# Optimization experiments

Measured on AMD Instinct MI355X. Metric: run time of the kernel, lower is better.

## Reference

```python
import jax, jax.numpy as jnp
import numpy as np

E, H, F, LE, LD, K, CD, DIN = 256, 8, 1024, 4, 3, 8, 4, 4
B, S = 16, 512
SIG2 = 1.0 ** 2 + 1e-8   # dr_sigma**2 + 1e-8
EPS = 1e-5               # LayerNorm / BatchNorm eps


def _ln(x, w, b):
    m = x.mean(-1, keepdims=True)
    v = ((x - m) ** 2).mean(-1, keepdims=True)
    return (x - m) / jnp.sqrt(v + EPS) * w + b


def _gelu(x):
    return jax.nn.gelu(x, approximate=False)  # torch nn.GELU default = exact erf


def _mha(xq, xkv, qkv_w, qkv_b, out_w, out_b, bias=None):
    # torch nn.MultiheadAttention (batch_first), additive float attn bias broadcast over heads
    wq, wk, wv = jnp.split(qkv_w, 3, axis=0)
    bq, bk, bv = jnp.split(qkv_b, 3)
    q = xq @ wq.T + bq
    k = xkv @ wk.T + bk
    v = xkv @ wv.T + bv
    Bn, Tq, Tk = q.shape[0], q.shape[1], k.shape[1]
    hd = E // H
    qh = q.reshape(Bn, Tq, H, hd)
    kh = k.reshape(Bn, Tk, H, hd)
    vh = v.reshape(Bn, Tk, H, hd)
    s = jnp.einsum('bqhd,bkhd->bhqk', qh, kh) / jnp.sqrt(jnp.asarray(hd, q.dtype))
    if bias is not None:
        s = s + bias[:, None]  # same bias for every head
    p = jax.nn.softmax(s, axis=-1)
    o = jnp.einsum('bhqk,bkhd->bqhd', p, vh).reshape(Bn, Tq, E)
    return o @ out_w.T + out_b


def _forward(x, mask, parent_idx, in_w, in_b, bn_w, bn_b, dr_gamma,
             e_qkv_w, e_qkv_b, e_out_w, e_out_b, e_l1_w, e_l1_b, e_l2_w, e_l2_b,
             e_n1_w, e_n1_b, e_n2_w, e_n2_b,
             parent_w, parent_b, query_embed, c1_w, c1_b, c2_w, c2_b,
             d_sqkv_w, d_sqkv_b, d_sout_w, d_sout_b,
             d_cqkv_w, d_cqkv_b, d_cout_w, d_cout_b,
             d_l1_w, d_l1_b, d_l2_w, d_l2_b,
             d_n1_w, d_n1_b, d_n2_w, d_n2_b, d_n3_w, d_n3_b,
             child_w, child_b, o1_w, o1_b, o2_w, o2_b):
    x = jnp.nan_to_num(x)
    # input_dim==4 convention: (log_pt, dEta, dPhi, log_E)
    coords = jnp.stack([x[..., 1], x[..., 2]], axis=-1)          # [B,S,2]
    # input_proj: Linear -> BatchNorm1d (eval: mean 0, var 1) -> GELU (dropout=identity in eval)
    h = x @ in_w.T + in_b
    h = (h / jnp.sqrt(1.0 + EPS)) * bn_w + bn_b
    h = _gelu(h)
    # dR Gaussian attention bias: [B,S,S]; mask is all-valid so no -inf fill
    d = coords[:, :, None, :] - coords[:, None, :, :]
    dr2 = d[..., 0] ** 2 + d[..., 1] ** 2
    bias = -(dr_gamma[0] * dr2) / (2.0 * SIG2)
    # dR-biased pre-norm encoder
    for i in range(LE):
        hn = _ln(h, e_n1_w[i], e_n1_b[i])
        h = h + _mha(hn, hn, e_qkv_w[i], e_qkv_b[i], e_out_w[i], e_out_b[i], bias)
        hn = _ln(h, e_n2_w[i], e_n2_b[i])
        h = h + _gelu(hn @ e_l1_w[i].T + e_l1_b[i]) @ e_l2_w[i].T + e_l2_b[i]
    memory = jnp.nan_to_num(h)
    parent_logit = (memory @ parent_w.T + parent_b)[..., 0]       # [B,S]
    # conditional decoder queries
    p = memory[jnp.arange(memory.shape[0]), parent_idx]           # [B,E]
    m = mask.astype(memory.dtype)
    g = (memory * m[..., None]).sum(1) / jnp.maximum(m.sum(1, keepdims=True), 1.0)
    cond = _gelu(jnp.concatenate([p, g], -1) @ c1_w.T + c1_b) @ c2_w.T + c2_b
    t = query_embed[None] + cond[:, None]                         # [B,K,E]
    # pre-norm transformer decoder (self-attn, cross-attn, ff)
    for i in range(LD):
        tn = _ln(t, d_n1_w[i], d_n1_b[i])
        t = t + _mha(tn, tn, d_sqkv_w[i], d_sqkv_b[i], d_sout_w[i], d_sout_b[i])
        tn = _ln(t, d_n2_w[i], d_n2_b[i])
        t = t + _mha(tn, memory, d_cqkv_w[i], d_cqkv_b[i], d_cout_w[i], d_cout_b[i])
        tn = _ln(t, d_n3_w[i], d_n3_b[i])
        t = t + _gelu(tn @ d_l1_w[i].T + d_l1_b[i]) @ d_l2_w[i].T + d_l2_b[i]
    child_feat = t @ child_w.T + child_b                          # [B,K,CD]
    obj_logit = (_gelu(t @ o1_w.T + o1_b) @ o2_w.T + o2_b)[..., 0]  # [B,K]
    return parent_logit, child_feat, obj_logit


def setup_inputs() -> dict:
    key = jax.random.key(0)
    ks = iter(jax.random.split(key, 64))
    def w(shape, scale=0.05):
        return jax.random.normal(next(ks), shape, jnp.float32) * scale
    return {
        'x': jax.random.normal(next(ks), (B, S, DIN), jnp.float32),
        'mask': jnp.ones((B, S), dtype=bool),
        'parent_idx': jax.random.randint(next(ks), (B,), 0, S),
        'in_w': w((E, DIN)), 'in_b': jnp.zeros((E,)),
        'bn_w': jnp.ones((E,)), 'bn_b': jnp.zeros((E,)),
        'dr_gamma': jnp.ones((1,)),
        'e_qkv_w': w((LE, 3 * E, E)), 'e_qkv_b': jnp.zeros((LE, 3 * E)),
        'e_out_w': w((LE, E, E)), 'e_out_b': jnp.zeros((LE, E)),
        'e_l1_w': w((LE, F, E)), 'e_l1_b': jnp.zeros((LE, F)),
        'e_l2_w': w((LE, E, F)), 'e_l2_b': jnp.zeros((LE, E)),
        'e_n1_w': jnp.ones((LE, E)), 'e_n1_b': jnp.zeros((LE, E)),
        'e_n2_w': jnp.ones((LE, E)), 'e_n2_b': jnp.zeros((LE, E)),
        'parent_w': w((1, E)), 'parent_b': jnp.zeros((1,)),
        'query_embed': w((K, E), 0.02),
        'c1_w': w((E, 2 * E)), 'c1_b': jnp.zeros((E,)),
        'c2_w': w((E, E)), 'c2_b': jnp.zeros((E,)),
        'd_sqkv_w': w((LD, 3 * E, E)), 'd_sqkv_b': jnp.zeros((LD, 3 * E)),
        'd_sout_w': w((LD, E, E)), 'd_sout_b': jnp.zeros((LD, E)),
        'd_cqkv_w': w((LD, 3 * E, E)), 'd_cqkv_b': jnp.zeros((LD, 3 * E)),
        'd_cout_w': w((LD, E, E)), 'd_cout_b': jnp.zeros((LD, E)),
        'd_l1_w': w((LD, F, E)), 'd_l1_b': jnp.zeros((LD, F)),
        'd_l2_w': w((LD, E, F)), 'd_l2_b': jnp.zeros((LD, E)),
        'd_n1_w': jnp.ones((LD, E)), 'd_n1_b': jnp.zeros((LD, E)),
        'd_n2_w': jnp.ones((LD, E)), 'd_n2_b': jnp.zeros((LD, E)),
        'd_n3_w': jnp.ones((LD, E)), 'd_n3_b': jnp.zeros((LD, E)),
        'child_w': w((CD, E)), 'child_b': jnp.zeros((CD,)),
        'o1_w': w((E, E)), 'o1_b': jnp.zeros((E,)),
        'o2_w': w((1, E)), 'o2_b': jnp.zeros((1,)),
    }


def reference(x, mask, parent_idx, in_w, in_b, bn_w, bn_b, dr_gamma,
              e_qkv_w, e_qkv_b, e_out_w, e_out_b, e_l1_w, e_l1_b, e_l2_w, e_l2_b,
              e_n1_w, e_n1_b, e_n2_w, e_n2_b,
              parent_w, parent_b, query_embed, c1_w, c1_b, c2_w, c2_b,
              d_sqkv_w, d_sqkv_b, d_sout_w, d_sout_b,
              d_cqkv_w, d_cqkv_b, d_cout_w, d_cout_b,
              d_l1_w, d_l1_b, d_l2_w, d_l2_b,
              d_n1_w, d_n1_b, d_n2_w, d_n2_b, d_n3_w, d_n3_b,
              child_w, child_b, o1_w, o1_b, o2_w, o2_b):
    return _forward(x, mask, parent_idx, in_w, in_b, bn_w, bn_b, dr_gamma,
                    e_qkv_w, e_qkv_b, e_out_w, e_out_b, e_l1_w, e_l1_b, e_l2_w, e_l2_b,
                    e_n1_w, e_n1_b, e_n2_w, e_n2_b,
                    parent_w, parent_b, query_embed, c1_w, c1_b, c2_w, c2_b,
                    d_sqkv_w, d_sqkv_b, d_sout_w, d_sout_b,
                    d_cqkv_w, d_cqkv_b, d_cout_w, d_cout_b,
                    d_l1_w, d_l1_b, d_l2_w, d_l2_b,
                    d_n1_w, d_n1_b, d_n2_w, d_n2_b, d_n3_w, d_n3_b,
                    child_w, child_b, o1_w, o1_b, o2_w, o2_b)
```

## Files before the change

kernel.cpp:

```cpp
#include <hip/hip_runtime.h>
#include <math.h>

#define E 256
#define H 8
#define HD 32
#define FF 1024
#define LE 4
#define LDN 3
#define KQ 8
#define CDIM 4
#define DIN 4
#define BATCH 16
#define SEQ 512

typedef __attribute__((ext_vector_type(8))) short s8b;
typedef __attribute__((ext_vector_type(4))) float f32x4;

__device__ __forceinline__ float gelu_f(float x) {
  return 0.5f * x * (1.f + erff(x * 0.70710678118654752f));
}

__device__ __forceinline__ unsigned short f2b(float f) {
  union { float f; unsigned u; } a;
  a.f = f;
  unsigned r = (a.u + 0x7fffu + ((a.u >> 16) & 1u)) >> 16;
  return (unsigned short)r;
}

__device__ __forceinline__ float b2f(unsigned short u) {
  union { unsigned u; float f; } a;
  a.u = ((unsigned)u) << 16;
  return a.f;
}

__device__ __forceinline__ void gload16(const unsigned short* g, unsigned short* l) {
  __builtin_amdgcn_global_load_lds((const __attribute__((address_space(1))) void*)g,
                                   (__attribute__((address_space(3))) void*)l, 16, 0, 0);
}

template <int GELU, int RESID, int OMODE>
__global__ __launch_bounds__(256) void mfma_gemm_kernel(
    const unsigned short* __restrict__ A, const unsigned short* __restrict__ Wt,
    const float* __restrict__ bias, const float* __restrict__ resid,
    float* __restrict__ outf, unsigned short* __restrict__ outb,
    unsigned short* __restrict__ vtb,
    int M, int N, int K) {
  __shared__ __align__(16) unsigned short As[128 * 32];
  __shared__ __align__(16) unsigned short Bs[128 * 32];
  int tid = threadIdx.x;
  int lane = tid & 63, w = tid >> 6;
  int row0 = blockIdx.y * 128, col0 = blockIdx.x * 128;
  int wr = (w >> 1) * 64, wc = (w & 1) * 64;
  f32x4 acc[4][4] = {};

  int sr0 = w * 32 + (lane >> 2);
  int sr1 = sr0 + 16;
  int sc = lane & 3;
  int gc0 = (sc ^ ((sr0 >> 1) & 3)) * 8;
  int gc1 = (sc ^ ((sr1 >> 1) & 3)) * 8;
  const unsigned short* Ap0 = A + (size_t)(row0 + sr0) * K + gc0;
  const unsigned short* Ap1 = A + (size_t)(row0 + sr1) * K + gc1;
  const unsigned short* Bp0 = Wt + (size_t)(col0 + sr0) * K + gc0;
  const unsigned short* Bp1 = Wt + (size_t)(col0 + sr1) * K + gc1;
  unsigned short* lA0 = As + (w * 32) * 32;
  unsigned short* lA1 = As + (w * 32 + 16) * 32;
  unsigned short* lB0 = Bs + (w * 32) * 32;
  unsigned short* lB1 = Bs + (w * 32 + 16) * 32;

  for (int k0 = 0; k0 < K; k0 += 32) {
    __syncthreads();
    gload16(Ap0 + k0, lA0);
    gload16(Ap1 + k0, lA1);
    gload16(Bp0 + k0, lB0);
    gload16(Bp1 + k0, lB1);
    __syncthreads();
    int krow = lane & 15, kq = lane >> 4;
    s8b afr[4], bfr[4];
    #pragma unroll
    for (int mi = 0; mi < 4; ++mi) {
      int r = wr + mi * 16 + krow;
      afr[mi] = *(const s8b*)(As + r * 32 + ((kq ^ ((r >> 1) & 3)) * 8));
    }
    #pragma unroll
    for (int ni = 0; ni < 4; ++ni) {
      int r = wc + ni * 16 + krow;
      bfr[ni] = *(const s8b*)(Bs + r * 32 + ((kq ^ ((r >> 1) & 3)) * 8));
    }
    #pragma unroll
    for (int mi = 0; mi < 4; ++mi)
      #pragma unroll
      for (int ni = 0; ni < 4; ++ni)
        acc[mi][ni] = __builtin_amdgcn_mfma_f32_16x16x32_bf16(afr[mi], bfr[ni], acc[mi][ni], 0, 0, 0);
  }

  int cl = lane & 15, rb = (lane >> 4) * 4;
  #pragma unroll
  for (int ni = 0; ni < 4; ++ni) {
    int col = col0 + wc + ni * 16 + cl;
    float bv = bias[col];
    #pragma unroll
    for (int mi = 0; mi < 4; ++mi) {
      #pragma unroll
      for (int j = 0; j < 4; ++j) {
        int row = row0 + wr + mi * 16 + rb + j;
        float v = acc[mi][ni][j] + bv;
        if (RESID) v += resid[(size_t)row * N + col];
        if (GELU) v = gelu_f(v);
        if (OMODE == 0) {
          outf[(size_t)row * N + col] = v;
        } else if (OMODE == 1) {
          outb[(size_t)row * N + col] = f2b(v);
        } else {
          int b = row >> 9, s = row & 511;
          int sect = col >> 8, hh = (col >> 5) & 7, d = col & 31;
          if (sect < 2)
            outb[((((size_t)sect * BATCH + b) * H + hh) * SEQ + s) * HD + d] = f2b(v);
          else
            vtb[(((size_t)b * H + hh) * HD + d) * SEQ + s] = f2b(v);
        }
      }
    }
  }
}

__global__ __launch_bounds__(256) void mfma_gemm64_kernel(
    const unsigned short* __restrict__ A, const unsigned short* __restrict__ Wt,
    const float* __restrict__ bias, const float* __restrict__ resid,
    float* __restrict__ outf, int M, int N, int K) {
  __shared__ __align__(16) unsigned short As[64 * 32];
  __shared__ __align__(16) unsigned short Bs[128 * 32];
  int tid = threadIdx.x;
  int lane = tid & 63, w = tid >> 6;
  int row0 = blockIdx.y * 64, col0 = blockIdx.x * 128;
  int wr = (w >> 1) * 32, wc = (w & 1) * 64;
  f32x4 acc[2][4] = {};

  int sc = lane & 3;
  int srA = w * 16 + (lane >> 2);
  int gcA = (sc ^ ((srA >> 1) & 3)) * 8;
  const unsigned short* ApA = A + (size_t)(row0 + srA) * K + gcA;
  unsigned short* lA = As + (w * 16) * 32;
  int sr0 = w * 32 + (lane >> 2);
  int sr1 = sr0 + 16;
  int gc0 = (sc ^ ((sr0 >> 1) & 3)) * 8;
  int gc1 = (sc ^ ((sr1 >> 1) & 3)) * 8;
  const unsigned short* Bp0 = Wt + (size_t)(col0 + sr0) * K + gc0;
  const unsigned short* Bp1 = Wt + (size_t)(col0 + sr1) * K + gc1;
  unsigned short* lB0 = Bs + (w * 32) * 32;
  unsigned short* lB1 = Bs + (w * 32 + 16) * 32;

  for (int k0 = 0; k0 < K; k0 += 32) {
    __syncthreads();
    gload16(ApA + k0, lA);
    gload16(Bp0 + k0, lB0);
    gload16(Bp1 + k0, lB1);
    __syncthreads();
    int krow = lane & 15, kq = lane >> 4;
    s8b afr[2], bfr[4];
    #pragma unroll
    for (int mi = 0; mi < 2; ++mi) {
      int r = wr + mi * 16 + krow;
      afr[mi] = *(const s8b*)(As + r * 32 + ((kq ^ ((r >> 1) & 3)) * 8));
    }
    #pragma unroll
    for (int ni = 0; ni < 4; ++ni) {
      int r = wc + ni * 16 + krow;
      bfr[ni] = *(const s8b*)(Bs + r * 32 + ((kq ^ ((r >> 1) & 3)) * 8));
    }
    #pragma unroll
    for (int mi = 0; mi < 2; ++mi)
      #pragma unroll
      for (int ni = 0; ni < 4; ++ni)
        acc[mi][ni] = __builtin_amdgcn_mfma_f32_16x16x32_bf16(afr[mi], bfr[ni], acc[mi][ni], 0, 0, 0);
  }

  int cl = lane & 15, rb = (lane >> 4) * 4;
  #pragma unroll
  for (int ni = 0; ni < 4; ++ni) {
    int col = col0 + wc + ni * 16 + cl;
    float bv = bias[col];
    #pragma unroll
    for (int mi = 0; mi < 2; ++mi) {
      #pragma unroll
      for (int j = 0; j < 4; ++j) {
        int row = row0 + wr + mi * 16 + rb + j;
        float v = acc[mi][ni][j] + bv + resid[(size_t)row * N + col];
        outf[(size_t)row * N + col] = v;
      }
    }
  }
}

__global__ __launch_bounds__(256) void mfma_attn_kernel(
    const unsigned short* __restrict__ qkb, const unsigned short* __restrict__ vt,
    const float2* __restrict__ carr, const float* __restrict__ gamma_p,
    unsigned short* __restrict__ out) {
  __shared__ __align__(16) unsigned short P[4][16 * 64];
  int tid = threadIdx.x, lane = tid & 63, w = tid >> 6;
  int qt = blockIdx.x, h = blockIdx.y, b = blockIdx.z;
  int q0 = qt * 64 + w * 16;
  const unsigned short* qh = qkb + (((size_t)b * H + h) * SEQ) * HD;
  const unsigned short* kh = qkb + ((((size_t)BATCH + b) * H + h) * SEQ) * HD;
  const unsigned short* vh = vt + (((size_t)b * H + h) * HD) * SEQ;
  int r16 = lane & 15, q4 = lane >> 4;
  s8b qa = *(const s8b*)(qh + (size_t)(q0 + r16) * HD + q4 * 8);
  float eq[4], pq[4];
  #pragma unroll
  for (int j = 0; j < 4; ++j) {
    float2 c = carr[b * SEQ + q0 + q4 * 4 + j];
    eq[j] = c.x; pq[j] = c.y;
  }
  float gam = gamma_p[0] * 0.49999999500000004f;
  const float scale = 0.17677669529663687f;
  float m[4], lsum[4];
  #pragma unroll
  for (int j = 0; j < 4; ++j) { m[j] = -1e30f; lsum[j] = 0.f; }
  f32x4 o0 = {}, o1 = {};
  const f32x4 zf = {0.f, 0.f, 0.f, 0.f};
  unsigned short* pw = &P[w][0];

  for (int t = 0; t < SEQ / 64; ++t) {
    int k0 = t * 64;
    f32x4 sf[4];
    #pragma unroll
    for (int f = 0; f < 4; ++f) {
      s8b bk = *(const s8b*)(kh + (size_t)(k0 + f * 16 + r16) * HD + q4 * 8);
      sf[f] = __builtin_amdgcn_mfma_f32_16x16x32_bf16(qa, bk, zf, 0, 0, 0);
    }
    float ek[4], pk[4];
    #pragma unroll
    for (int f = 0; f < 4; ++f) {
      float2 c = carr[b * SEQ + k0 + f * 16 + r16];
      ek[f] = c.x; pk[f] = c.y;
    }
    float sc_[4][4];
    float tmax[4] = {-1e30f, -1e30f, -1e30f, -1e30f};
    #pragma unroll
    for (int f = 0; f < 4; ++f)
      #pragma unroll
      for (int j = 0; j < 4; ++j) {
        float de = eq[j] - ek[f], dp = pq[j] - pk[f];
        float v = sf[f][j] * scale - gam * (de * de + dp * dp);
        sc_[f][j] = v;
        tmax[j] = fmaxf(tmax[j], v);
      }
    #pragma unroll
    for (int j = 0; j < 4; ++j) {
      #pragma unroll
      for (int off = 1; off < 16; off <<= 1)
        tmax[j] = fmaxf(tmax[j], __shfl_xor(tmax[j], off));
      float mn = fmaxf(m[j], tmax[j]);
      float al = __expf(m[j] - mn);
      m[j] = mn;
      lsum[j] *= al;
      o0[j] *= al;
      o1[j] *= al;
    }
    __syncthreads();
    #pragma unroll
    for (int f = 0; f < 4; ++f)
      #pragma unroll
      for (int j = 0; j < 4; ++j) {
        float p = __expf(sc_[f][j] - m[j]);
        lsum[j] += p;
        int prow = q4 * 4 + j;
        int c = f * 16 + r16;
        int chunk = (c >> 3) ^ (prow & 7);
        pw[prow * 64 + chunk * 8 + (c & 7)] = f2b(p);
      }
    __syncthreads();
    #pragma unroll
    for (int ks = 0; ks < 2; ++ks) {
      int chunk = (ks * 4 + q4) ^ (r16 & 7);
      s8b pa = *(const s8b*)(pw + r16 * 64 + chunk * 8);
      s8b v0 = *(const s8b*)(vh + (size_t)r16 * SEQ + k0 + ks * 32 + q4 * 8);
      s8b v1 = *(const s8b*)(vh + (size_t)(16 + r16) * SEQ + k0 + ks * 32 + q4 * 8);
      o0 = __builtin_amdgcn_mfma_f32_16x16x32_bf16(pa, v0, o0, 0, 0, 0);
      o1 = __builtin_amdgcn_mfma_f32_16x16x32_bf16(pa, v1, o1, 0, 0, 0);
    }
  }
  #pragma unroll
  for (int j = 0; j < 4; ++j) {
    #pragma unroll
    for (int off = 1; off < 16; off <<= 1)
      lsum[j] += __shfl_xor(lsum[j], off);
    float inv = 1.f / lsum[j];
    size_t rbase = ((size_t)(b * SEQ + q0 + q4 * 4 + j)) * E + h * HD;
    out[rbase + r16] = f2b(o0[j] * inv);
    out[rbase + 16 + r16] = f2b(o1[j] * inv);
  }
}

__global__ void coords_kernel(const float* __restrict__ x, float2* __restrict__ carr) {
  int i = blockIdx.x * 256 + threadIdx.x;
  if (i >= BATCH * SEQ) return;
  carr[i] = make_float2(x[(size_t)i * DIN + 1], x[(size_t)i * DIN + 2]);
}

__global__ void f2b_kernel(const float* __restrict__ in, unsigned short* __restrict__ out, int n4) {
  int i = blockIdx.x * 256 + threadIdx.x;
  if (i >= n4) return;
  float4 v = ((const float4*)in)[i];
  ushort4 o;
  o.x = f2b(v.x); o.y = f2b(v.y); o.z = f2b(v.z); o.w = f2b(v.w);
  ((ushort4*)out)[i] = o;
}

__global__ void kvw_remap_kernel(const float* __restrict__ w, const float* __restrict__ b,
                                 unsigned short* __restrict__ wout, float* __restrict__ bout) {
  int i = blockIdx.x * 256 + threadIdx.x;
  if (i < 1536) bout[i] = b[(i >> 9) * 768 + 256 + (i & 511)];
  if (i >= 98304) return;
  int row = i >> 6, cc = i & 63;
  int l = row >> 9, rr = row & 511;
  const float* src = w + ((size_t)l * 768 + 256 + rr) * 256 + cc * 4;
  float4 v = *(const float4*)src;
  ushort4 o;
  o.x = f2b(v.x); o.y = f2b(v.y); o.z = f2b(v.z); o.w = f2b(v.w);
  *(ushort4*)(wout + (size_t)row * 256 + cc * 4) = o;
}


template <int N, int GELU>
__global__ __launch_bounds__(256) void dec_ln_gemv_kernel(
    const float* __restrict__ t, const float* __restrict__ nw, const float* __restrict__ nb,
    const float* __restrict__ W, const float* __restrict__ bias, float* __restrict__ outg) {
  __shared__ float X[8][256];
  __shared__ float Pp[4][64][9];
  int b = blockIdx.x, by = blockIdx.y, tid = threadIdx.x;
  const float* tg = t + (size_t)b * 2048;
  int w = tid >> 6, l = tid & 63;
  #pragma unroll
  for (int rr = 0; rr < 2; ++rr) {
    int r = w * 2 + rr;
    float v0 = tg[r * 256 + l], v1 = tg[r * 256 + 64 + l];
    float v2 = tg[r * 256 + 128 + l], v3 = tg[r * 256 + 192 + l];
    float s = v0 + v1 + v2 + v3;
    for (int o = 32; o > 0; o >>= 1) s += __shfl_xor(s, o);
    float mean = s * (1.f / 256);
    float d0 = v0 - mean, d1 = v1 - mean, d2 = v2 - mean, d3 = v3 - mean;
    float var = d0 * d0 + d1 * d1 + d2 * d2 + d3 * d3;
    for (int o = 32; o > 0; o >>= 1) var += __shfl_xor(var, o);
    float inv = rsqrtf(var * (1.f / 256) + 1e-5f);
    X[r][l] = d0 * inv * nw[l] + nb[l];
    X[r][l + 64] = d1 * inv * nw[l + 64] + nb[l + 64];
    X[r][l + 128] = d2 * inv * nw[l + 128] + nb[l + 128];
    X[r][l + 192] = d3 * inv * nw[l + 192] + nb[l + 192];
  }
  __syncthreads();
  int j = tid & 63, kq = tid >> 6;
  int col = by * 64 + j;
  const float4* wp = (const float4*)(W + (size_t)col * 256 + kq * 64);
  float acc[8] = {};
  #pragma unroll
  for (int kk = 0; kk < 16; ++kk) {
    float4 wv = wp[kk];
    int base = kq * 64 + kk * 4;
    #pragma unroll
    for (int r = 0; r < 8; ++r) {
      float4 xv = *(const float4*)&X[r][base];
      acc[r] += xv.x * wv.x + xv.y * wv.y + xv.z * wv.z + xv.w * wv.w;
    }
  }
  #pragma unroll
  for (int r = 0; r < 8; ++r) Pp[kq][j][r] = acc[r];
  __syncthreads();
  for (int i = tid; i < 512; i += 256) {
    int r = i & 7, j2 = i >> 3;
    float v = Pp[0][j2][r] + Pp[1][j2][r] + Pp[2][j2][r] + Pp[3][j2][r] + bias[by * 64 + j2];
    if (GELU) v = gelu_f(v);
    outg[((size_t)b * 8 + r) * N + by * 64 + j2] = v;
  }
}

__global__ __launch_bounds__(256) void dec_selfattn_sout_kernel(
    const float* __restrict__ qkvg, const float* __restrict__ W, const float* __restrict__ bias,
    float* __restrict__ t) {
  __shared__ float QK[8][768];
  __shared__ float S[512];
  __shared__ float X[8][256];
  __shared__ float Pp[4][64][9];
  int b = blockIdx.x, by = blockIdx.y, tid = threadIdx.x;
  const float* qg = qkvg + (size_t)b * 8 * 768;
  for (int i = tid; i < 6144; i += 256) ((float*)QK)[i] = qg[i];
  __syncthreads();
  for (int t2 = tid; t2 < 512; t2 += 256) {
    int h = t2 >> 6, q = (t2 >> 3) & 7, k = t2 & 7;
    const float* qp = &QK[q][h * 32];
    const float* kp = &QK[k][256 + h * 32];
    float d = 0.f;
    #pragma unroll
    for (int jj = 0; jj < 32; ++jj) d += qp[jj] * kp[jj];
    S[t2] = d * 0.17677669529663687f;
  }
  __syncthreads();
  if (tid < 64) {
    float* row = &S[tid * 8];
    float m = row[0];
    #pragma unroll
    for (int k = 1; k < 8; ++k) m = fmaxf(m, row[k]);
    float sum = 0.f;
    #pragma unroll
    for (int k = 0; k < 8; ++k) { float e = __expf(row[k] - m); row[k] = e; sum += e; }
    float inv = 1.f / sum;
    #pragma unroll
    for (int k = 0; k < 8; ++k) row[k] *= inv;
  }
  __syncthreads();
  for (int i = tid; i < 2048; i += 256) {
    int q = i >> 8, c = i & 255, h = c >> 5;
    const float* pr = &S[h * 64 + q * 8];
    float acc = 0.f;
    #pragma unroll
    for (int k = 0; k < 8; ++k) acc += pr[k] * QK[k][512 + c];
    X[q][c] = acc;
  }
  __syncthreads();
  int j = tid & 63, kq = tid >> 6;
  int col = by * 64 + j;
  const float4* wp = (const float4*)(W + (size_t)col * 256 + kq * 64);
  float acc[8] = {};
  #pragma unroll
  for (int kk = 0; kk < 16; ++kk) {
    float4 wv = wp[kk];
    int base = kq * 64 + kk * 4;
    #pragma unroll
    for (int r = 0; r < 8; ++r) {
      float4 xv = *(const float4*)&X[r][base];
      acc[r] += xv.x * wv.x + xv.y * wv.y + xv.z * wv.z + xv.w * wv.w;
    }
  }
  #pragma unroll
  for (int r = 0; r < 8; ++r) Pp[kq][j][r] = acc[r];
  __syncthreads();
  for (int i = tid; i < 512; i += 256) {
    int r = i & 7, j2 = i >> 3;
    float v = Pp[0][j2][r] + Pp[1][j2][r] + Pp[2][j2][r] + Pp[3][j2][r] + bias[by * 64 + j2];
    t[((size_t)b * 8 + r) * 256 + by * 64 + j2] += v;
  }
}

__global__ __launch_bounds__(256) void dec_gemv_resid_kernel(
    const float* __restrict__ Xg, const float* __restrict__ W, const float* __restrict__ bias,
    float* __restrict__ t) {
  __shared__ float X[8][256];
  __shared__ float Pp[4][64][9];
  int b = blockIdx.x, by = blockIdx.y, tid = threadIdx.x;
  const float* xg = Xg + (size_t)b * 2048;
  for (int i = tid; i < 2048; i += 256) ((float*)X)[i] = xg[i];
  __syncthreads();
  int j = tid & 63, kq = tid >> 6;
  int col = by * 64 + j;
  const float4* wp = (const float4*)(W + (size_t)col * 256 + kq * 64);
  float acc[8] = {};
  #pragma unroll
  for (int kk = 0; kk < 16; ++kk) {
    float4 wv = wp[kk];
    int base = kq * 64 + kk * 4;
    #pragma unroll
    for (int r = 0; r < 8; ++r) {
      float4 xv = *(const float4*)&X[r][base];
      acc[r] += xv.x * wv.x + xv.y * wv.y + xv.z * wv.z + xv.w * wv.w;
    }
  }
  #pragma unroll
  for (int r = 0; r < 8; ++r) Pp[kq][j][r] = acc[r];
  __syncthreads();
  for (int i = tid; i < 512; i += 256) {
    int r = i & 7, j2 = i >> 3;
    float v = Pp[0][j2][r] + Pp[1][j2][r] + Pp[2][j2][r] + Pp[3][j2][r] + bias[by * 64 + j2];
    t[((size_t)b * 8 + r) * 256 + by * 64 + j2] += v;
  }
}

__global__ __launch_bounds__(256) void dec_ffn2_kernel(
    const float* __restrict__ MIDg, const float* __restrict__ W, const float* __restrict__ bias,
    float* __restrict__ t) {
  __shared__ float X[8][1024];
  __shared__ float Pp[4][64][9];
  int b = blockIdx.x, by = blockIdx.y, tid = threadIdx.x;
  const float* xg = MIDg + (size_t)b * 8192;
  for (int i = tid; i < 8192; i += 256) ((float*)X)[i] = xg[i];
  __syncthreads();
  int j = tid & 63, kq = tid >> 6;
  int col = by * 64 + j;
  const float4* wp = (const float4*)(W + (size_t)col * 1024 + kq * 256);
  float acc[8] = {};
  #pragma unroll 8
  for (int kk = 0; kk < 64; ++kk) {
    float4 wv = wp[kk];
    int base = kq * 256 + kk * 4;
    #pragma unroll
    for (int r = 0; r < 8; ++r) {
      float4 xv = *(const float4*)&X[r][base];
      acc[r] += xv.x * wv.x + xv.y * wv.y + xv.z * wv.z + xv.w * wv.w;
    }
  }
  #pragma unroll
  for (int r = 0; r < 8; ++r) Pp[kq][j][r] = acc[r];
  __syncthreads();
  for (int i = tid; i < 512; i += 256) {
    int r = i & 7, j2 = i >> 3;
    float v = Pp[0][j2][r] + Pp[1][j2][r] + Pp[2][j2][r] + Pp[3][j2][r] + bias[by * 64 + j2];
    t[((size_t)b * 8 + r) * 256 + by * 64 + j2] += v;
  }
}

__global__ __launch_bounds__(256) void cross_attn_kernel(
    const float* __restrict__ Q, const unsigned short* __restrict__ KV,
    int koff, int voff, float* __restrict__ out) {
  __shared__ float sv[512];
  __shared__ float red[256];
  __shared__ float qv[32];
  __shared__ float pvred[8][32];
  int tid = threadIdx.x;
  int bid = blockIdx.x;
  int q = bid % KQ;
  int h = (bid / KQ) % H;
  int b = bid / (KQ * H);
  if (tid < 32) qv[tid] = Q[((size_t)(b * KQ + q)) * E + h * HD + tid];
  __syncthreads();
  const float scale = 0.17677669529663687f;
  for (int k = tid; k < SEQ; k += 256) {
    const unsigned short* kp = KV + ((size_t)(b * SEQ + k)) * 1536 + koff + h * HD;
    float d = 0.f;
    #pragma unroll
    for (int j4 = 0; j4 < 4; ++j4) {
      s8b kv8 = *(const s8b*)(kp + j4 * 8);
      #pragma unroll
      for (int j = 0; j < 8; ++j)
        d += qv[j4 * 8 + j] * b2f((unsigned short)kv8[j]);
    }
    sv[k] = d * scale;
  }
  __syncthreads();
  float m = -1e30f;
  for (int k = tid; k < SEQ; k += 256) m = fmaxf(m, sv[k]);
  red[tid] = m; __syncthreads();
  for (int s = 128; s > 0; s >>= 1) {
    if (tid < s) red[tid] = fmaxf(red[tid], red[tid + s]);
    __syncthreads();
  }
  m = red[0]; __syncthreads();
  float lsum = 0.f;
  for (int k = tid; k < SEQ; k += 256) { float e = __expf(sv[k] - m); sv[k] = e; lsum += e; }
  red[tid] = lsum; __syncthreads();
  for (int s = 128; s > 0; s >>= 1) {
    if (tid < s) red[tid] += red[tid + s];
    __syncthreads();
  }
  float denom = red[0];
  int d = tid & 31, g = tid >> 5;
  float acc = 0.f;
  for (int k = g; k < SEQ; k += 8)
    acc += sv[k] * b2f(KV[((size_t)(b * SEQ + k)) * 1536 + voff + h * HD + d]);
  pvred[g][d] = acc;
  __syncthreads();
  if (tid < 32) {
    float r = 0.f;
    #pragma unroll
    for (int gg = 0; gg < 8; ++gg) r += pvred[gg][tid];
    out[((size_t)(b * KQ + q)) * E + h * HD + tid] = r / denom;
  }
}

__global__ void ln_bf16_kernel(const float* __restrict__ in, const float* __restrict__ w,
                               const float* __restrict__ b, unsigned short* __restrict__ out) {
  int r = blockIdx.x;
  int l = threadIdx.x;
  const float* p = in + (size_t)r * E;
  float v0 = p[l], v1 = p[l + 64], v2 = p[l + 128], v3 = p[l + 192];
  float s = v0 + v1 + v2 + v3;
  for (int off = 32; off > 0; off >>= 1) s += __shfl_xor(s, off);
  float mean = s * (1.f / E);
  float d0 = v0 - mean, d1 = v1 - mean, d2 = v2 - mean, d3 = v3 - mean;
  float var = d0 * d0 + d1 * d1 + d2 * d2 + d3 * d3;
  for (int off = 32; off > 0; off >>= 1) var += __shfl_xor(var, off);
  float inv = rsqrtf(var * (1.f / E) + 1e-5f);
  unsigned short* o = out + (size_t)r * E;
  o[l]       = f2b(d0 * inv * w[l]       + b[l]);
  o[l + 64]  = f2b(d1 * inv * w[l + 64]  + b[l + 64]);
  o[l + 128] = f2b(d2 * inv * w[l + 128] + b[l + 128]);
  o[l + 192] = f2b(d3 * inv * w[l + 192] + b[l + 192]);
}

__global__ void input_proj_kernel(const float* __restrict__ x, const float* __restrict__ in_w,
                                  const float* __restrict__ in_b, const float* __restrict__ bn_w,
                                  const float* __restrict__ bn_b, float* __restrict__ h) {
  int idx = blockIdx.x * 256 + threadIdx.x;
  int row = idx >> 8, e = idx & 255;
  const float* xr = x + (size_t)row * DIN;
  float v = in_b[e];
  #pragma unroll
  for (int i = 0; i < DIN; ++i) v += xr[i] * in_w[e * DIN + i];
  v = v * (1.0f / sqrtf(1.0f + 1e-5f)) * bn_w[e] + bn_b[e];
  h[idx] = gelu_f(v);
}

__global__ __launch_bounds__(256) void pool_gather_kernel(
    const float* __restrict__ mem, const int* __restrict__ pidx, float* __restrict__ pg) {
  __shared__ float red[8][32];
  int b = blockIdx.x, cy = blockIdx.y, tid = threadIdx.x;
  int c = cy * 32 + (tid & 31), g = tid >> 5;
  float s = 0.f;
  for (int r = g; r < SEQ; r += 8)
    s += mem[((size_t)b * SEQ + r) * E + c];
  red[g][tid & 31] = s;
  __syncthreads();
  if (tid < 32) {
    float t = 0.f;
    #pragma unroll
    for (int g2 = 0; g2 < 8; ++g2) t += red[g2][tid];
    pg[(size_t)b * 512 + 256 + cy * 32 + tid] = t * (1.f / SEQ);
    pg[(size_t)b * 512 + cy * 32 + tid] = mem[((size_t)b * SEQ + pidx[b]) * E + cy * 32 + tid];
  }
}

__global__ void cond_kernel(const float* __restrict__ pg, const float* __restrict__ c1w,
                            const float* __restrict__ c1b, const float* __restrict__ c2w,
                            const float* __restrict__ c2b, const float* __restrict__ qe,
                            float* __restrict__ t) {
  __shared__ float PG[512];
  __shared__ float C1[256];
  int b = blockIdx.x, c = threadIdx.x;
  PG[c] = pg[(size_t)b * 512 + c];
  PG[c + 256] = pg[(size_t)b * 512 + 256 + c];
  __syncthreads();
  const float4* wp = (const float4*)(c1w + (size_t)c * 512);
  float acc = c1b[c];
  #pragma unroll 8
  for (int kk = 0; kk < 128; ++kk) {
    float4 wv = wp[kk];
    int base = kk * 4;
    acc += PG[base] * wv.x + PG[base + 1] * wv.y + PG[base + 2] * wv.z + PG[base + 3] * wv.w;
  }
  C1[c] = gelu_f(acc);
  __syncthreads();
  const float4* wp2 = (const float4*)(c2w + (size_t)c * 256);
  float acc2 = c2b[c];
  #pragma unroll 8
  for (int kk = 0; kk < 64; ++kk) {
    float4 wv = wp2[kk];
    int base = kk * 4;
    acc2 += C1[base] * wv.x + C1[base + 1] * wv.y + C1[base + 2] * wv.z + C1[base + 3] * wv.w;
  }
  #pragma unroll
  for (int k = 0; k < KQ; ++k)
    t[((size_t)b * KQ + k) * E + c] = qe[k * E + c] + acc2;
}

__global__ void head_kernel(const float* __restrict__ t,
                            const float* __restrict__ childw, const float* __restrict__ childb,
                            const float* __restrict__ o1w, const float* __restrict__ o1b,
                            const float* __restrict__ o2w, const float* __restrict__ o2b,
                            float* __restrict__ out_child, float* __restrict__ out_obj) {
  __shared__ float tr[256];
  __shared__ float red[256];
  int r = blockIdx.x, c = threadIdx.x;
  tr[c] = t[(size_t)r * E + c];
  __syncthreads();
  const float4* wp = (const float4*)(o1w + (size_t)c * 256);
  float acc = o1b[c];
  #pragma unroll 8
  for (int kk = 0; kk < 64; ++kk) {
    float4 wv = wp[kk];
    int base = kk * 4;
    acc += tr[base] * wv.x + tr[base + 1] * wv.y + tr[base + 2] * wv.z + tr[base + 3] * wv.w;
  }
  red[c] = gelu_f(acc) * o2w[c];
  __syncthreads();
  for (int s = 128; s > 0; s >>= 1) {
    if (c < s) red[c] += red[c + s];
    __syncthreads();
  }
  if (c == 0) out_obj[r] = red[0] + o2b[0];
  __syncthreads();
  #pragma unroll
  for (int j = 0; j < CDIM; ++j) {
    red[c] = tr[c] * childw[j * E + c];
    __syncthreads();
    for (int s = 128; s > 0; s >>= 1) {
      if (c < s) red[c] += red[c + s];
      __syncthreads();
    }
    if (c == 0) out_child[r * CDIM + j] = red[0] + childb[j];
    __syncthreads();
  }
}

__global__ void rowdot_kernel(const float* __restrict__ A, const float* __restrict__ w,
                              const float* __restrict__ bias, float* __restrict__ out) {
  int r = blockIdx.x, l = threadIdx.x;
  const float* p = A + (size_t)r * E;
  float s = p[l] * w[l] + p[l + 64] * w[l + 64] + p[l + 128] * w[l + 128] + p[l + 192] * w[l + 192];
  for (int off = 32; off > 0; off >>= 1) s += __shfl_xor(s, off);
  if (l == 0) out[r] = s + bias[0];
}

extern "C" void kernel_launch(void* const* d_in, const int* in_sizes, int n_in,
                              void* d_out, int out_size, void* d_ws, size_t ws_size,
                              hipStream_t stream) {
  const float* x          = (const float*)d_in[0];
  const int*   parent_idx = (const int*)d_in[2];
  const float* in_w  = (const float*)d_in[3];
  const float* in_b  = (const float*)d_in[4];
  const float* bn_w  = (const float*)d_in[5];
  const float* bn_b  = (const float*)d_in[6];
  const float* dr_gamma = (const float*)d_in[7];
  const float* e_qkv_w = (const float*)d_in[8];
  const float* e_qkv_b = (const float*)d_in[9];
  const float* e_out_w = (const float*)d_in[10];
  const float* e_out_b = (const float*)d_in[11];
  const float* e_l1_w = (const float*)d_in[12];
  const float* e_l1_b = (const float*)d_in[13];
  const float* e_l2_w = (const float*)d_in[14];
  const float* e_l2_b = (const float*)d_in[15];
  const float* e_n1_w = (const float*)d_in[16];
  const float* e_n1_b = (const float*)d_in[17];
  const float* e_n2_w = (const float*)d_in[18];
  const float* e_n2_b = (const float*)d_in[19];
  const float* parent_w = (const float*)d_in[20];
  const float* parent_b = (const float*)d_in[21];
  const float* query_embed = (const float*)d_in[22];
  const float* c1_w = (const float*)d_in[23];
  const float* c1_b = (const float*)d_in[24];
  const float* c2_w = (const float*)d_in[25];
  const float* c2_b = (const float*)d_in[26];
  const float* d_sqkv_w = (const float*)d_in[27];
  const float* d_sqkv_b = (const float*)d_in[28];
  const float* d_sout_w = (const float*)d_in[29];
  const float* d_sout_b = (const float*)d_in[30];
  const float* d_cqkv_w = (const float*)d_in[31];
  const float* d_cqkv_b = (const float*)d_in[32];
  const float* d_cout_w = (const float*)d_in[33];
  const float* d_cout_b = (const float*)d_in[34];
  const float* d_l1_w = (const float*)d_in[35];
  const float* d_l1_b = (const float*)d_in[36];
  const float* d_l2_w = (const float*)d_in[37];
  const float* d_l2_b = (const float*)d_in[38];
  const float* d_n1_w = (const float*)d_in[39];
  const float* d_n1_b = (const float*)d_in[40];
  const float* d_n2_w = (const float*)d_in[41];
  const float* d_n2_b = (const float*)d_in[42];
  const float* d_n3_w = (const float*)d_in[43];
  const float* d_n3_b = (const float*)d_in[44];
  const float* child_w = (const float*)d_in[45];
  const float* child_b = (const float*)d_in[46];
  const float* o1_w = (const float*)d_in[47];
  const float* o1_b = (const float*)d_in[48];
  const float* o2_w = (const float*)d_in[49];
  const float* o2_b = (const float*)d_in[50];

  float* out = (float*)d_out;
  const int ROWS = BATCH * SEQ;
  const int TROWS = BATCH * KQ;

  float* ws = (float*)d_ws;
  float* h         = ws;
  float* attnout_d = h + (size_t)ROWS * E;
  float* pg        = attnout_d + (size_t)TROWS * E;
  float* tbuf      = pg + BATCH * 2 * E;
  float* q_t       = tbuf + (size_t)TROWS * E;
  float* qkv_t     = q_t + (size_t)TROWS * E;
  float* dmid      = qkv_t + (size_t)TROWS * 3 * E;
  float* kvb3      = dmid + (size_t)TROWS * FF;
  unsigned short* kv_bf   = (unsigned short*)(kvb3 + 1536);
  unsigned short* hn_bf   = kv_bf + (size_t)ROWS * 1536;
  unsigned short* attn_bf = hn_bf + (size_t)ROWS * E;
  unsigned short* mid_bf  = attn_bf + (size_t)ROWS * E;
  unsigned short* eqkv_bf = mid_bf + (size_t)ROWS * FF;
  unsigned short* eout_bf = eqkv_bf + (size_t)LE * 3 * E * E;
  unsigned short* el1_bf  = eout_bf + (size_t)LE * E * E;
  unsigned short* el2_bf  = el1_bf + (size_t)LE * FF * E;
  unsigned short* kvw_bf  = el2_bf + (size_t)LE * E * FF;
  float2* carr = (float2*)(kvw_bf + (size_t)1536 * 256);
  unsigned short* qkb = mid_bf;
  unsigned short* vtb = mid_bf + (size_t)2 * ROWS * E;

  auto cvt = [&](const float* src, unsigned short* dst, size_t n) {
    int n4 = (int)(n / 4);
    f2b_kernel<<<(n4 + 255) / 256, 256, 0, stream>>>(src, dst, n4);
  };

  cvt(e_qkv_w, eqkv_bf, (size_t)LE * 3 * E * E);
  cvt(e_out_w, eout_bf, (size_t)LE * E * E);
  cvt(e_l1_w, el1_bf, (size_t)LE * FF * E);
  cvt(e_l2_w, el2_bf, (size_t)LE * E * FF);
  kvw_remap_kernel<<<384, 256, 0, stream>>>(d_cqkv_w, d_cqkv_b, kvw_bf, kvb3);
  coords_kernel<<<(BATCH * SEQ + 255) / 256, 256, 0, stream>>>(x, carr);

  input_proj_kernel<<<ROWS, 256, 0, stream>>>(x, in_w, in_b, bn_w, bn_b, h);

  for (int i = 0; i < LE; ++i) {
    const float* qb = e_qkv_b + (size_t)i * 3 * E;
    const float* ob = e_out_b + (size_t)i * E;
    const float* l1b = e_l1_b + (size_t)i * FF;
    const float* l2b = e_l2_b + (size_t)i * E;
    ln_bf16_kernel<<<ROWS, 64, 0, stream>>>(h, e_n1_w + i * E, e_n1_b + i * E, hn_bf);
    mfma_gemm_kernel<0, 0, 2><<<dim3(6, 64), 256, 0, stream>>>(
        hn_bf, eqkv_bf + (size_t)i * 3 * E * E, qb, nullptr, nullptr, qkb, vtb, ROWS, 3 * E, E);
    mfma_attn_kernel<<<dim3(SEQ / 64, H, BATCH), 256, 0, stream>>>(qkb, vtb, carr, dr_gamma, attn_bf);
    mfma_gemm64_kernel<<<dim3(2, 128), 256, 0, stream>>>(
        attn_bf, eout_bf + (size_t)i * E * E, ob, h, h, ROWS, E, E);
    ln_bf16_kernel<<<ROWS, 64, 0, stream>>>(h, e_n2_w + i * E, e_n2_b + i * E, hn_bf);
    mfma_gemm_kernel<1, 0, 1><<<dim3(8, 64), 256, 0, stream>>>(
        hn_bf, el1_bf + (size_t)i * FF * E, l1b, nullptr, nullptr, mid_bf, nullptr, ROWS, FF, E);
    mfma_gemm64_kernel<<<dim3(2, 128), 256, 0, stream>>>(
        mid_bf, el2_bf + (size_t)i * E * FF, l2b, h, h, ROWS, E, FF);
  }

  rowdot_kernel<<<ROWS, 64, 0, stream>>>(h, parent_w, parent_b, out);

  pool_gather_kernel<<<dim3(BATCH, 8), 256, 0, stream>>>(h, parent_idx, pg);
  cond_kernel<<<BATCH, 256, 0, stream>>>(pg, c1_w, c1_b, c2_w, c2_b, query_embed, tbuf);

  cvt(h, hn_bf, (size_t)ROWS * E);
  mfma_gemm_kernel<0, 0, 1><<<dim3(12, 64), 256, 0, stream>>>(
      hn_bf, kvw_bf, kvb3, nullptr, nullptr, kv_bf, nullptr, ROWS, 3 * E * 2, E);

  for (int i = 0; i < LDN; ++i) {
    dec_ln_gemv_kernel<768, 0><<<dim3(BATCH, 12), 256, 0, stream>>>(
        tbuf, d_n1_w + i * E, d_n1_b + i * E,
        d_sqkv_w + (size_t)i * 3 * E * E, d_sqkv_b + (size_t)i * 3 * E, qkv_t);
    dec_selfattn_sout_kernel<<<dim3(BATCH, 4), 256, 0, stream>>>(
        qkv_t, d_sout_w + (size_t)i * E * E, d_sout_b + (size_t)i * E, tbuf);
    dec_ln_gemv_kernel<256, 0><<<dim3(BATCH, 4), 256, 0, stream>>>(
        tbuf, d_n2_w + i * E, d_n2_b + i * E,
        d_cqkv_w + (size_t)i * 3 * E * E, d_cqkv_b + (size_t)i * 3 * E, q_t);
    cross_attn_kernel<<<BATCH * H * KQ, 256, 0, stream>>>(
        q_t, kv_bf, i * 512, i * 512 + 256, attnout_d);
    dec_gemv_resid_kernel<<<dim3(BATCH, 4), 256, 0, stream>>>(
        attnout_d, d_cout_w + (size_t)i * E * E, d_cout_b + (size_t)i * E, tbuf);
    dec_ln_gemv_kernel<1024, 1><<<dim3(BATCH, 16), 256, 0, stream>>>(
        tbuf, d_n3_w + i * E, d_n3_b + i * E,
        d_l1_w + (size_t)i * FF * E, d_l1_b + (size_t)i * FF, dmid);
    dec_ffn2_kernel<<<dim3(BATCH, 4), 256, 0, stream>>>(
        dmid, d_l2_w + (size_t)i * E * FF, d_l2_b + (size_t)i * E, tbuf);
  }

  head_kernel<<<TROWS, 256, 0, stream>>>(tbuf, child_w, child_b, o1_w, o1_b, o2_w, o2_b,
                                         out + ROWS, out + ROWS + TROWS * CDIM);
}
```

Measured before the change: 804.9 us.

## Fuse kernels, merge weight conversions, and use 64-row GEMM tiles everywhere

Combines four weight-conversion launches into one kernel, fuses the input projection with the first encoder LayerNorm, and fuses the decoder's LN plus cross-attention query projection into the cross-attention kernel. It also replaces the 128x128 GEMM with a 64x128 tile variant for the QKV, FFN1 and KV projections, doubling block count. Together these cut launch count and intermediate traffic and raise occupancy. The cost is that each cross-attention block recomputes the LN and a head's query projection redundantly, and the smaller tiles give less data reuse per block.

```diff
diff --git a/kernel.cpp b/kernel.cpp
--- a/kernel.cpp
+++ b/kernel.cpp
@@ -38,95 +38,11 @@
                                    (__attribute__((address_space(3))) void*)l, 16, 0, 0);
 }
 
-template <int GELU, int RESID, int OMODE>
-__global__ __launch_bounds__(256) void mfma_gemm_kernel(
+template <int GELU, int OMODE>
+__global__ __launch_bounds__(256) void mfma_gemm64o_kernel(
     const unsigned short* __restrict__ A, const unsigned short* __restrict__ Wt,
-    const float* __restrict__ bias, const float* __restrict__ resid,
-    float* __restrict__ outf, unsigned short* __restrict__ outb,
-    unsigned short* __restrict__ vtb,
-    int M, int N, int K) {
-  __shared__ __align__(16) unsigned short As[128 * 32];
-  __shared__ __align__(16) unsigned short Bs[128 * 32];
-  int tid = threadIdx.x;
-  int lane = tid & 63, w = tid >> 6;
-  int row0 = blockIdx.y * 128, col0 = blockIdx.x * 128;
-  int wr = (w >> 1) * 64, wc = (w & 1) * 64;
-  f32x4 acc[4][4] = {};
-
-  int sr0 = w * 32 + (lane >> 2);
-  int sr1 = sr0 + 16;
-  int sc = lane & 3;
-  int gc0 = (sc ^ ((sr0 >> 1) & 3)) * 8;
-  int gc1 = (sc ^ ((sr1 >> 1) & 3)) * 8;
-  const unsigned short* Ap0 = A + (size_t)(row0 + sr0) * K + gc0;
-  const unsigned short* Ap1 = A + (size_t)(row0 + sr1) * K + gc1;
-  const unsigned short* Bp0 = Wt + (size_t)(col0 + sr0) * K + gc0;
-  const unsigned short* Bp1 = Wt + (size_t)(col0 + sr1) * K + gc1;
-  unsigned short* lA0 = As + (w * 32) * 32;
-  unsigned short* lA1 = As + (w * 32 + 16) * 32;
-  unsigned short* lB0 = Bs + (w * 32) * 32;
-  unsigned short* lB1 = Bs + (w * 32 + 16) * 32;
-
-  for (int k0 = 0; k0 < K; k0 += 32) {
-    __syncthreads();
-    gload16(Ap0 + k0, lA0);
-    gload16(Ap1 + k0, lA1);
-    gload16(Bp0 + k0, lB0);
-    gload16(Bp1 + k0, lB1);
-    __syncthreads();
-    int krow = lane & 15, kq = lane >> 4;
-    s8b afr[4], bfr[4];
-    #pragma unroll
-    for (int mi = 0; mi < 4; ++mi) {
-      int r = wr + mi * 16 + krow;
-      afr[mi] = *(const s8b*)(As + r * 32 + ((kq ^ ((r >> 1) & 3)) * 8));
-    }
-    #pragma unroll
-    for (int ni = 0; ni < 4; ++ni) {
-      int r = wc + ni * 16 + krow;
-      bfr[ni] = *(const s8b*)(Bs + r * 32 + ((kq ^ ((r >> 1) & 3)) * 8));
-    }
-    #pragma unroll
-    for (int mi = 0; mi < 4; ++mi)
-      #pragma unroll
-      for (int ni = 0; ni < 4; ++ni)
-        acc[mi][ni] = __builtin_amdgcn_mfma_f32_16x16x32_bf16(afr[mi], bfr[ni], acc[mi][ni], 0, 0, 0);
-  }
-
-  int cl = lane & 15, rb = (lane >> 4) * 4;
-  #pragma unroll
-  for (int ni = 0; ni < 4; ++ni) {
-    int col = col0 + wc + ni * 16 + cl;
-    float bv = bias[col];
-    #pragma unroll
-    for (int mi = 0; mi < 4; ++mi) {
-      #pragma unroll
-      for (int j = 0; j < 4; ++j) {
-        int row = row0 + wr + mi * 16 + rb + j;
-        float v = acc[mi][ni][j] + bv;
-        if (RESID) v += resid[(size_t)row * N + col];
-        if (GELU) v = gelu_f(v);
-        if (OMODE == 0) {
-          outf[(size_t)row * N + col] = v;
-        } else if (OMODE == 1) {
-          outb[(size_t)row * N + col] = f2b(v);
-        } else {
-          int b = row >> 9, s = row & 511;
-          int sect = col >> 8, hh = (col >> 5) & 7, d = col & 31;
-          if (sect < 2)
-            outb[((((size_t)sect * BATCH + b) * H + hh) * SEQ + s) * HD + d] = f2b(v);
-          else
-            vtb[(((size_t)b * H + hh) * HD + d) * SEQ + s] = f2b(v);
-        }
-      }
-    }
-  }
-}
-
-__global__ __launch_bounds__(256) void mfma_gemm64_kernel(
-    const unsigned short* __restrict__ A, const unsigned short* __restrict__ Wt,
-    const float* __restrict__ bias, const float* __restrict__ resid,
-    float* __restrict__ outf, int M, int N, int K) {
+    const float* __restrict__ bias, unsigned short* __restrict__ outb,
+    unsigned short* __restrict__ vtb, int N, int K) {
   __shared__ __align__(16) unsigned short As[64 * 32];
   __shared__ __align__(16) unsigned short Bs[128 * 32];
   int tid = threadIdx.x;
@@ -184,8 +100,85 @@
       #pragma unroll
       for (int j = 0; j < 4; ++j) {
         int row = row0 + wr + mi * 16 + rb + j;
-        float v = acc[mi][ni][j] + bv + resid[(size_t)row * N + col];
-        outf[(size_t)row * N + col] = v;
+        float v = acc[mi][ni][j] + bv;
+        if (GELU) v = gelu_f(v);
+        if (OMODE == 1) {
+          outb[(size_t)row * N + col] = f2b(v);
+        } else {
+          int b = row >> 9, s = row & 511;
+          int sect = col >> 8, hh = (col >> 5) & 7, d = col & 31;
+          if (sect < 2)
+            outb[((((size_t)sect * BATCH + b) * H + hh) * SEQ + s) * HD + d] = f2b(v);
+          else
+            vtb[(((size_t)b * H + hh) * HD + d) * SEQ + s] = f2b(v);
+        }
+      }
+    }
+  }
+}
+
+__global__ __launch_bounds__(256) void mfma_gemm64_kernel(
+    const unsigned short* __restrict__ A, const unsigned short* __restrict__ Wt,
+    const float* __restrict__ bias, const float* __restrict__ resid,
+    float* __restrict__ outf, int M, int N, int K) {
+  __shared__ __align__(16) unsigned short As[64 * 32];
+  __shared__ __align__(16) unsigned short Bs[128 * 32];
+  int tid = threadIdx.x;
+  int lane = tid & 63, w = tid >> 6;
+  int row0 = blockIdx.y * 64, col0 = blockIdx.x * 128;
+  int wr = (w >> 1) * 32, wc = (w & 1) * 64;
+  f32x4 acc[2][4] = {};
+
+  int sc = lane & 3;
+  int srA = w * 16 + (lane >> 2);
+  int gcA = (sc ^ ((srA >> 1) & 3)) * 8;
+  const unsigned short* ApA = A + (size_t)(row0 + srA) * K + gcA;
+  unsigned short* lA = As + (w * 16) * 32;
+  int sr0 = w * 32 + (lane >> 2);
+  int sr1 = sr0 + 16;
+  int gc0 = (sc ^ ((sr0 >> 1) & 3)) * 8;
+  int gc1 = (sc ^ ((sr1 >> 1) & 3)) * 8;
+  const unsigned short* Bp0 = Wt + (size_t)(col0 + sr0) * K + gc0;
+  const unsigned short* Bp1 = Wt + (size_t)(col0 + sr1) * K + gc1;
+  unsigned short* lB0 = Bs + (w * 32) * 32;
+  unsigned short* lB1 = Bs + (w * 32 + 16) * 32;
+
+  for (int k0 = 0; k0 < K; k0 += 32) {
+    __syncthreads();
+    gload16(ApA + k0, lA);
+    gload16(Bp0 + k0, lB0);
+    gload16(Bp1 + k0, lB1);
+    __syncthreads();
+    int krow = lane & 15, kq = lane >> 4;
+    s8b afr[2], bfr[4];
+    #pragma unroll
+    for (int mi = 0; mi < 2; ++mi) {
+      int r = wr + mi * 16 + krow;
+      afr[mi] = *(const s8b*)(As + r * 32 + ((kq ^ ((r >> 1) & 3)) * 8));
+    }
+    #pragma unroll
+    for (int ni = 0; ni < 4; ++ni) {
+      int r = wc + ni * 16 + krow;
+      bfr[ni] = *(const s8b*)(Bs + r * 32 + ((kq ^ ((r >> 1) & 3)) * 8));
+    }
+    #pragma unroll
+    for (int mi = 0; mi < 2; ++mi)
+      #pragma unroll
+      for (int ni = 0; ni < 4; ++ni)
+        acc[mi][ni] = __builtin_amdgcn_mfma_f32_16x16x32_bf16(afr[mi], bfr[ni], acc[mi][ni], 0, 0, 0);
+  }
+
+  int cl = lane & 15, rb = (lane >> 4) * 4;
+  #pragma unroll
+  for (int ni = 0; ni < 4; ++ni) {
+    int col = col0 + wc + ni * 16 + cl;
+    float bv = bias[col];
+    #pragma unroll
+    for (int mi = 0; mi < 2; ++mi) {
+      #pragma unroll
+      for (int j = 0; j < 4; ++j) {
+        int row = row0 + wr + mi * 16 + rb + j;
+        outf[(size_t)row * N + col] = acc[mi][ni][j] + bv + resid[(size_t)row * N + col];
       }
     }
   }
@@ -306,6 +299,25 @@
   ((ushort4*)out)[i] = o;
 }
 
+__global__ void cvt_all_kernel(const float* __restrict__ w0, const float* __restrict__ w1,
+                               const float* __restrict__ w2, const float* __restrict__ w3,
+                               unsigned short* __restrict__ o0, unsigned short* __restrict__ o1,
+                               unsigned short* __restrict__ o2, unsigned short* __restrict__ o3) {
+  const int n0 = LE * 3 * E * E / 4, n1 = LE * E * E / 4;
+  const int n2 = LE * FF * E / 4, n3 = LE * E * FF / 4;
+  int j = blockIdx.x * 256 + threadIdx.x;
+  const float* src; unsigned short* dst;
+  if (j < n0) { src = w0; dst = o0; }
+  else if ((j -= n0) < n1) { src = w1; dst = o1; }
+  else if ((j -= n1) < n2) { src = w2; dst = o2; }
+  else if ((j -= n2) < n3) { src = w3; dst = o3; }
+  else return;
+  float4 v = ((const float4*)src)[j];
+  ushort4 o;
+  o.x = f2b(v.x); o.y = f2b(v.y); o.z = f2b(v.z); o.w = f2b(v.w);
+  ((ushort4*)dst)[j] = o;
+}
+
 __global__ void kvw_remap_kernel(const float* __restrict__ w, const float* __restrict__ b,
                                  unsigned short* __restrict__ wout, float* __restrict__ bout) {
   int i = blockIdx.x * 256 + threadIdx.x;
@@ -320,248 +332,36 @@
   *(ushort4*)(wout + (size_t)row * 256 + cc * 4) = o;
 }
 
-
-template <int N, int GELU>
-__global__ __launch_bounds__(256) void dec_ln_gemv_kernel(
-    const float* __restrict__ t, const float* __restrict__ nw, const float* __restrict__ nb,
-    const float* __restrict__ W, const float* __restrict__ bias, float* __restrict__ outg) {
-  __shared__ float X[8][256];
-  __shared__ float Pp[4][64][9];
-  int b = blockIdx.x, by = blockIdx.y, tid = threadIdx.x;
-  const float* tg = t + (size_t)b * 2048;
-  int w = tid >> 6, l = tid & 63;
-  #pragma unroll
-  for (int rr = 0; rr < 2; ++rr) {
-    int r = w * 2 + rr;
-    float v0 = tg[r * 256 + l], v1 = tg[r * 256 + 64 + l];
-    float v2 = tg[r * 256 + 128 + l], v3 = tg[r * 256 + 192 + l];
-    float s = v0 + v1 + v2 + v3;
-    for (int o = 32; o > 0; o >>= 1) s += __shfl_xor(s, o);
-    float mean = s * (1.f / 256);
-    float d0 = v0 - mean, d1 = v1 - mean, d2 = v2 - mean, d3 = v3 - mean;
-    float var = d0 * d0 + d1 * d1 + d2 * d2 + d3 * d3;
-    for (int o = 32; o > 0; o >>= 1) var += __shfl_xor(var, o);
-    float inv = rsqrtf(var * (1.f / 256) + 1e-5f);
-    X[r][l] = d0 * inv * nw[l] + nb[l];
-    X[r][l + 64] = d1 * inv * nw[l + 64] + nb[l + 64];
-    X[r][l + 128] = d2 * inv * nw[l + 128] + nb[l + 128];
-    X[r][l + 192] = d3 * inv * nw[l + 192] + nb[l + 192];
-  }
-  __syncthreads();
-  int j = tid & 63, kq = tid >> 6;
-  int col = by * 64 + j;
-  const float4* wp = (const float4*)(W + (size_t)col * 256 + kq * 64);
-  float acc[8] = {};
-  #pragma unroll
-  for (int kk = 0; kk < 16; ++kk) {
-    float4 wv = wp[kk];
-    int base = kq * 64 + kk * 4;
-    #pragma unroll
-    for (int r = 0; r < 8; ++r) {
-      float4 xv = *(const float4*)&X[r][base];
-      acc[r] += xv.x * wv.x + xv.y * wv.y + xv.z * wv.z + xv.w * wv.w;
-    }
-  }
-  #pragma unroll
-  for (int r = 0; r < 8; ++r) Pp[kq][j][r] = acc[r];
-  __syncthreads();
-  for (int i = tid; i < 512; i += 256) {
-    int r = i & 7, j2 = i >> 3;
-    float v = Pp[0][j2][r] + Pp[1][j2][r] + Pp[2][j2][r] + Pp[3][j2][r] + bias[by * 64 + j2];
-    if (GELU) v = gelu_f(v);
-    outg[((size_t)b * 8 + r) * N + by * 64 + j2] = v;
-  }
-}
-
-__global__ __launch_bounds__(256) void dec_selfattn_sout_kernel(
-    const float* __restrict__ qkvg, const float* __restrict__ W, const float* __restrict__ bias,
-    float* __restrict__ t) {
-  __shared__ float QK[8][768];
-  __shared__ float S[512];
-  __shared__ float X[8][256];
-  __shared__ float Pp[4][64][9];
-  int b = blockIdx.x, by = blockIdx.y, tid = threadIdx.x;
-  const float* qg = qkvg + (size_t)b * 8 * 768;
-  for (int i = tid; i < 6144; i += 256) ((float*)QK)[i] = qg[i];
-  __syncthreads();
-  for (int t2 = tid; t2 < 512; t2 += 256) {
-    int h = t2 >> 6, q = (t2 >> 3) & 7, k = t2 & 7;
-    const float* qp = &QK[q][h * 32];
-    const float* kp = &QK[k][256 + h * 32];
-    float d = 0.f;
-    #pragma unroll
-    for (int jj = 0; jj < 32; ++jj) d += qp[jj] * kp[jj];
-    S[t2] = d * 0.17677669529663687f;
-  }
-  __syncthreads();
-  if (tid < 64) {
-    float* row = &S[tid * 8];
-    float m = row[0];
-    #pragma unroll
-    for (int k = 1; k < 8; ++k) m = fmaxf(m, row[k]);
-    float sum = 0.f;
-    #pragma unroll
-    for (int k = 0; k < 8; ++k) { float e = __expf(row[k] - m); row[k] = e; sum += e; }
-    float inv = 1.f / sum;
-    #pragma unroll
-    for (int k = 0; k < 8; ++k) row[k] *= inv;
-  }
-  __syncthreads();
-  for (int i = tid; i < 2048; i += 256) {
-    int q = i >> 8, c = i & 255, h = c >> 5;
-    const float* pr = &S[h * 64 + q * 8];
-    float acc = 0.f;
-    #pragma unroll
-    for (int k = 0; k < 8; ++k) acc += pr[k] * QK[k][512 + c];
-    X[q][c] = acc;
-  }
-  __syncthreads();
-  int j = tid & 63, kq = tid >> 6;
-  int col = by * 64 + j;
-  const float4* wp = (const float4*)(W + (size_t)col * 256 + kq * 64);
-  float acc[8] = {};
-  #pragma unroll
-  for (int kk = 0; kk < 16; ++kk) {
-    float4 wv = wp[kk];
-    int base = kq * 64 + kk * 4;
-    #pragma unroll
-    for (int r = 0; r < 8; ++r) {
-      float4 xv = *(const float4*)&X[r][base];
-      acc[r] += xv.x * wv.x + xv.y * wv.y + xv.z * wv.z + xv.w * wv.w;
-    }
-  }
-  #pragma unroll
-  for (int r = 0; r < 8; ++r) Pp[kq][j][r] = acc[r];
-  __syncthreads();
-  for (int i = tid; i < 512; i += 256) {
-    int r = i & 7, j2 = i >> 3;
-    float v = Pp[0][j2][r] + Pp[1][j2][r] + Pp[2][j2][r] + Pp[3][j2][r] + bias[by * 64 + j2];
-    t[((size_t)b * 8 + r) * 256 + by * 64 + j2] += v;
-  }
-}
-
-__global__ __launch_bounds__(256) void dec_gemv_resid_kernel(
-    const float* __restrict__ Xg, const float* __restrict__ W, const float* __restrict__ bias,
-    float* __restrict__ t) {
-  __shared__ float X[8][256];
-  __shared__ float Pp[4][64][9];
-  int b = blockIdx.x, by = blockIdx.y, tid = threadIdx.x;
-  const float* xg = Xg + (size_t)b * 2048;
-  for (int i = tid; i < 2048; i += 256) ((float*)X)[i] = xg[i];
-  __syncthreads();
-  int j = tid & 63, kq = tid >> 6;
-  int col = by * 64 + j;
-  const float4* wp = (const float4*)(W + (size_t)col * 256 + kq * 64);
-  float acc[8] = {};
-  #pragma unroll
-  for (int kk = 0; kk < 16; ++kk) {
-    float4 wv = wp[kk];
-    int base = kq * 64 + kk * 4;
-    #pragma unroll
-    for (int r = 0; r < 8; ++r) {
-      float4 xv = *(const float4*)&X[r][base];
-      acc[r] += xv.x * wv.x + xv.y * wv.y + xv.z * wv.z + xv.w * wv.w;
-    }
-  }
-  #pragma unroll
-  for (int r = 0; r < 8; ++r) Pp[kq][j][r] = acc[r];
-  __syncthreads();
-  for (int i = tid; i < 512; i += 256) {
-    int r = i & 7, j2 = i >> 3;
-    float v = Pp[0][j2][r] + Pp[1][j2][r] + Pp[2][j2][r] + Pp[3][j2][r] + bias[by * 64 + j2];
-    t[((size_t)b * 8 + r) * 256 + by * 64 + j2] += v;
-  }
-}
-
-__global__ __launch_bounds__(256) void dec_ffn2_kernel(
-    const float* __restrict__ MIDg, const float* __restrict__ W, const float* __restrict__ bias,
-    float* __restrict__ t) {
-  __shared__ float X[8][1024];
-  __shared__ float Pp[4][64][9];
-  int b = blockIdx.x, by = blockIdx.y, tid = threadIdx.x;
-  const float* xg = MIDg + (size_t)b * 8192;
-  for (int i = tid; i < 8192; i += 256) ((float*)X)[i] = xg[i];
-  __syncthreads();
-  int j = tid & 63, kq = tid >> 6;
-  int col = by * 64 + j;
-  const float4* wp = (const float4*)(W + (size_t)col * 1024 + kq * 256);
-  float acc[8] = {};
-  #pragma unroll 8
-  for (int kk = 0; kk < 64; ++kk) {
-    float4 wv = wp[kk];
-    int base = kq * 256 + kk * 4;
-    #pragma unroll
-    for (int r = 0; r < 8; ++r) {
-      float4 xv = *(const float4*)&X[r][base];
-      acc[r] += xv.x * wv.x + xv.y * wv.y + xv.z * wv.z + xv.w * wv.w;
-    }
-  }
-  #pragma unroll
-  for (int r = 0; r < 8; ++r) Pp[kq][j][r] = acc[r];
-  __syncthreads();
-  for (int i = tid; i < 512; i += 256) {
-    int r = i & 7, j2 = i >> 3;
-    float v = Pp[0][j2][r] + Pp[1][j2][r] + Pp[2][j2][r] + Pp[3][j2][r] + bias[by * 64 + j2];
-    t[((size_t)b * 8 + r) * 256 + by * 64 + j2] += v;
-  }
-}
-
-__global__ __launch_bounds__(256) void cross_attn_kernel(
-    const float* __restrict__ Q, const unsigned short* __restrict__ KV,
-    int koff, int voff, float* __restrict__ out) {
-  __shared__ float sv[512];
-  __shared__ float red[256];
-  __shared__ float qv[32];
-  __shared__ float pvred[8][32];
-  int tid = threadIdx.x;
-  int bid = blockIdx.x;
-  int q = bid % KQ;
-  int h = (bid / KQ) % H;
-  int b = bid / (KQ * H);
-  if (tid < 32) qv[tid] = Q[((size_t)(b * KQ + q)) * E + h * HD + tid];
-  __syncthreads();
-  const float scale = 0.17677669529663687f;
-  for (int k = tid; k < SEQ; k += 256) {
-    const unsigned short* kp = KV + ((size_t)(b * SEQ + k)) * 1536 + koff + h * HD;
-    float d = 0.f;
-    #pragma unroll
-    for (int j4 = 0; j4 < 4; ++j4) {
-      s8b kv8 = *(const s8b*)(kp + j4 * 8);
-      #pragma unroll
-      for (int j = 0; j < 8; ++j)
-        d += qv[j4 * 8 + j] * b2f((unsigned short)kv8[j]);
-    }
-    sv[k] = d * scale;
-  }
-  __syncthreads();
-  float m = -1e30f;
-  for (int k = tid; k < SEQ; k += 256) m = fmaxf(m, sv[k]);
-  red[tid] = m; __syncthreads();
-  for (int s = 128; s > 0; s >>= 1) {
-    if (tid < s) red[tid] = fmaxf(red[tid], red[tid + s]);
-    __syncthreads();
-  }
-  m = red[0]; __syncthreads();
-  float lsum = 0.f;
-  for (int k = tid; k < SEQ; k += 256) { float e = __expf(sv[k] - m); sv[k] = e; lsum += e; }
-  red[tid] = lsum; __syncthreads();
-  for (int s = 128; s > 0; s >>= 1) {
-    if (tid < s) red[tid] += red[tid + s];
-    __syncthreads();
-  }
-  float denom = red[0];
-  int d = tid & 31, g = tid >> 5;
-  float acc = 0.f;
-  for (int k = g; k < SEQ; k += 8)
-    acc += sv[k] * b2f(KV[((size_t)(b * SEQ + k)) * 1536 + voff + h * HD + d]);
-  pvred[g][d] = acc;
-  __syncthreads();
-  if (tid < 32) {
-    float r = 0.f;
-    #pragma unroll
-    for (int gg = 0; gg < 8; ++gg) r += pvred[gg][tid];
-    out[((size_t)(b * KQ + q)) * E + h * HD + tid] = r / denom;
-  }
+__global__ __launch_bounds__(256) void input_proj_ln_kernel(
+    const float* __restrict__ x, const float* __restrict__ in_w, const float* __restrict__ in_b,
+    const float* __restrict__ bn_w, const float* __restrict__ bn_b,
+    const float* __restrict__ nw, const float* __restrict__ nb,
+    float* __restrict__ h, unsigned short* __restrict__ hn) {
+  __shared__ float sred[4];
+  __shared__ float vred[4];
+  int row = blockIdx.x, e = threadIdx.x;
+  const float* xr = x + (size_t)row * DIN;
+  float v = in_b[e];
+  #pragma unroll
+  for (int i = 0; i < DIN; ++i) v += xr[i] * in_w[e * DIN + i];
+  v = v * (1.0f / sqrtf(1.0f + 1e-5f)) * bn_w[e] + bn_b[e];
+  v = gelu_f(v);
+  h[(size_t)row * 256 + e] = v;
+  int lane = e & 63, w = e >> 6;
+  float s = v;
+  #pragma unroll
+  for (int off = 32; off > 0; off >>= 1) s += __shfl_xor(s, off);
+  if (lane == 0) sred[w] = s;
+  __syncthreads();
+  float mean = (sred[0] + sred[1] + sred[2] + sred[3]) * (1.f / 256);
+  float d = v - mean;
+  float vr = d * d;
+  #pragma unroll
+  for (int off = 32; off > 0; off >>= 1) vr += __shfl_xor(vr, off);
+  if (lane == 0) vred[w] = vr;
+  __syncthreads();
+  float inv = rsqrtf((vred[0] + vred[1] + vred[2] + vred[3]) * (1.f / 256) + 1e-5f);
+  hn[(size_t)row * 256 + e] = f2b(d * inv * nw[e] + nb[e]);
 }
 
 __global__ void ln_bf16_kernel(const float* __restrict__ in, const float* __restrict__ w,
@@ -584,17 +384,289 @@
   o[l + 192] = f2b(d3 * inv * w[l + 192] + b[l + 192]);
 }
 
-__global__ void input_proj_kernel(const float* __restrict__ x, const float* __restrict__ in_w,
-                                  const float* __restrict__ in_b, const float* __restrict__ bn_w,
-                                  const float* __restrict__ bn_b, float* __restrict__ h) {
-  int idx = blockIdx.x * 256 + threadIdx.x;
-  int row = idx >> 8, e = idx & 255;
-  const float* xr = x + (size_t)row * DIN;
-  float v = in_b[e];
-  #pragma unroll
-  for (int i = 0; i < DIN; ++i) v += xr[i] * in_w[e * DIN + i];
-  v = v * (1.0f / sqrtf(1.0f + 1e-5f)) * bn_w[e] + bn_b[e];
-  h[idx] = gelu_f(v);
+
+template <int N, int GELU>
+__global__ __launch_bounds__(256) void dec_ln_gemv_kernel(
+    const float* __restrict__ t, const float* __restrict__ nw, const float* __restrict__ nb,
+    const float* __restrict__ W, const float* __restrict__ bias, float* __restrict__ outg) {
+  __shared__ float X[8][256];
+  __shared__ float Pp[4][64][9];
+  int b = blockIdx.x, by = blockIdx.y, tid = threadIdx.x;
+  const float* tg = t + (size_t)b * 2048;
+  int w = tid >> 6, l = tid & 63;
+  #pragma unroll
+  for (int rr = 0; rr < 2; ++rr) {
+    int r = w * 2 + rr;
+    float v0 = tg[r * 256 + l], v1 = tg[r * 256 + 64 + l];
+    float v2 = tg[r * 256 + 128 + l], v3 = tg[r * 256 + 192 + l];
+    float s = v0 + v1 + v2 + v3;
+    for (int o = 32; o > 0; o >>= 1) s += __shfl_xor(s, o);
+    float mean = s * (1.f / 256);
+    float d0 = v0 - mean, d1 = v1 - mean, d2 = v2 - mean, d3 = v3 - mean;
+    float var = d0 * d0 + d1 * d1 + d2 * d2 + d3 * d3;
+    for (int o = 32; o > 0; o >>= 1) var += __shfl_xor(var, o);
+    float inv = rsqrtf(var * (1.f / 256) + 1e-5f);
+    X[r][l] = d0 * inv * nw[l] + nb[l];
+    X[r][l + 64] = d1 * inv * nw[l + 64] + nb[l + 64];
+    X[r][l + 128] = d2 * inv * nw[l + 128] + nb[l + 128];
+    X[r][l + 192] = d3 * inv * nw[l + 192] + nb[l + 192];
+  }
+  __syncthreads();
+  int j = tid & 63, kq = tid >> 6;
+  int col = by * 64 + j;
+  const float4* wp = (const float4*)(W + (size_t)col * 256 + kq * 64);
+  float acc[8] = {};
+  #pragma unroll
+  for (int kk = 0; kk < 16; ++kk) {
+    float4 wv = wp[kk];
+    int base = kq * 64 + kk * 4;
+    #pragma unroll
+    for (int r = 0; r < 8; ++r) {
+      float4 xv = *(const float4*)&X[r][base];
+      acc[r] += xv.x * wv.x + xv.y * wv.y + xv.z * wv.z + xv.w * wv.w;
+    }
+  }
+  #pragma unroll
+  for (int r = 0; r < 8; ++r) Pp[kq][j][r] = acc[r];
+  __syncthreads();
+  for (int i = tid; i < 512; i += 256) {
+    int r = i & 7, j2 = i >> 3;
+    float v = Pp[0][j2][r] + Pp[1][j2][r] + Pp[2][j2][r] + Pp[3][j2][r] + bias[by * 64 + j2];
+    if (GELU) v = gelu_f(v);
+    outg[((size_t)b * 8 + r) * N + by * 64 + j2] = v;
+  }
+}
+
+__global__ __launch_bounds__(256) void dec_selfattn_sout_kernel(
+    const float* __restrict__ qkvg, const float* __restrict__ W, const float* __restrict__ bias,
+    float* __restrict__ t) {
+  __shared__ float QK[8][768];
+  __shared__ float S[512];
+  __shared__ float X[8][256];
+  __shared__ float Pp[4][64][9];
+  int b = blockIdx.x, by = blockIdx.y, tid = threadIdx.x;
+  const float* qg = qkvg + (size_t)b * 8 * 768;
+  for (int i = tid; i < 6144; i += 256) ((float*)QK)[i] = qg[i];
+  __syncthreads();
+  for (int t2 = tid; t2 < 512; t2 += 256) {
+    int h = t2 >> 6, q = (t2 >> 3) & 7, k = t2 & 7;
+    const float* qp = &QK[q][h * 32];
+    const float* kp = &QK[k][256 + h * 32];
+    float d = 0.f;
+    #pragma unroll
+    for (int jj = 0; jj < 32; ++jj) d += qp[jj] * kp[jj];
+    S[t2] = d * 0.17677669529663687f;
+  }
+  __syncthreads();
+  if (tid < 64) {
+    float* row = &S[tid * 8];
+    float m = row[0];
+    #pragma unroll
+    for (int k = 1; k < 8; ++k) m = fmaxf(m, row[k]);
+    float sum = 0.f;
+    #pragma unroll
+    for (int k = 0; k < 8; ++k) { float e = __expf(row[k] - m); row[k] = e; sum += e; }
+    float inv = 1.f / sum;
+    #pragma unroll
+    for (int k = 0; k < 8; ++k) row[k] *= inv;
+  }
+  __syncthreads();
+  for (int i = tid; i < 2048; i += 256) {
+    int q = i >> 8, c = i & 255, h = c >> 5;
+    const float* pr = &S[h * 64 + q * 8];
+    float acc = 0.f;
+    #pragma unroll
+    for (int k = 0; k < 8; ++k) acc += pr[k] * QK[k][512 + c];
+    X[q][c] = acc;
+  }
+  __syncthreads();
+  int j = tid & 63, kq = tid >> 6;
+  int col = by * 64 + j;
+  const float4* wp = (const float4*)(W + (size_t)col * 256 + kq * 64);
+  float acc[8] = {};
+  #pragma unroll
+  for (int kk = 0; kk < 16; ++kk) {
+    float4 wv = wp[kk];
+    int base = kq * 64 + kk * 4;
+    #pragma unroll
+    for (int r = 0; r < 8; ++r) {
+      float4 xv = *(const float4*)&X[r][base];
+      acc[r] += xv.x * wv.x + xv.y * wv.y + xv.z * wv.z + xv.w * wv.w;
+    }
+  }
+  #pragma unroll
+  for (int r = 0; r < 8; ++r) Pp[kq][j][r] = acc[r];
+  __syncthreads();
+  for (int i = tid; i < 512; i += 256) {
+    int r = i & 7, j2 = i >> 3;
+    float v = Pp[0][j2][r] + Pp[1][j2][r] + Pp[2][j2][r] + Pp[3][j2][r] + bias[by * 64 + j2];
+    t[((size_t)b * 8 + r) * 256 + by * 64 + j2] += v;
+  }
+}
+
+__global__ __launch_bounds__(256) void dec_gemv_resid_kernel(
+    const float* __restrict__ Xg, const float* __restrict__ W, const float* __restrict__ bias,
+    float* __restrict__ t) {
+  __shared__ float X[8][256];
+  __shared__ float Pp[4][64][9];
+  int b = blockIdx.x, by = blockIdx.y, tid = threadIdx.x;
+  const float* xg = Xg + (size_t)b * 2048;
+  for (int i = tid; i < 2048; i += 256) ((float*)X)[i] = xg[i];
+  __syncthreads();
+  int j = tid & 63, kq = tid >> 6;
+  int col = by * 64 + j;
+  const float4* wp = (const float4*)(W + (size_t)col * 256 + kq * 64);
+  float acc[8] = {};
+  #pragma unroll
+  for (int kk = 0; kk < 16; ++kk) {
+    float4 wv = wp[kk];
+    int base = kq * 64 + kk * 4;
+    #pragma unroll
+    for (int r = 0; r < 8; ++r) {
+      float4 xv = *(const float4*)&X[r][base];
+      acc[r] += xv.x * wv.x + xv.y * wv.y + xv.z * wv.z + xv.w * wv.w;
+    }
+  }
+  #pragma unroll
+  for (int r = 0; r < 8; ++r) Pp[kq][j][r] = acc[r];
+  __syncthreads();
+  for (int i = tid; i < 512; i += 256) {
+    int r = i & 7, j2 = i >> 3;
+    float v = Pp[0][j2][r] + Pp[1][j2][r] + Pp[2][j2][r] + Pp[3][j2][r] + bias[by * 64 + j2];
+    t[((size_t)b * 8 + r) * 256 + by * 64 + j2] += v;
+  }
+}
+
+__global__ __launch_bounds__(256) void dec_ffn2_kernel(
+    const float* __restrict__ MIDg, const float* __restrict__ W, const float* __restrict__ bias,
+    float* __restrict__ t) {
+  __shared__ float X[8][1024];
+  __shared__ float Pp[4][64][9];
+  int b = blockIdx.x, by = blockIdx.y, tid = threadIdx.x;
+  const float* xg = MIDg + (size_t)b * 8192;
+  for (int i = tid; i < 8192; i += 256) ((float*)X)[i] = xg[i];
+  __syncthreads();
+  int j = tid & 63, kq = tid >> 6;
+  int col = by * 64 + j;
+  const float4* wp = (const float4*)(W + (size_t)col * 1024 + kq * 256);
+  float acc[8] = {};
+  #pragma unroll 8
+  for (int kk = 0; kk < 64; ++kk) {
+    float4 wv = wp[kk];
+    int base = kq * 256 + kk * 4;
+    #pragma unroll
+    for (int r = 0; r < 8; ++r) {
+      float4 xv = *(const float4*)&X[r][base];
+      acc[r] += xv.x * wv.x + xv.y * wv.y + xv.z * wv.z + xv.w * wv.w;
+    }
+  }
+  #pragma unroll
+  for (int r = 0; r < 8; ++r) Pp[kq][j][r] = acc[r];
+  __syncthreads();
+  for (int i = tid; i < 512; i += 256) {
+    int r = i & 7, j2 = i >> 3;
+    float v = Pp[0][j2][r] + Pp[1][j2][r] + Pp[2][j2][r] + Pp[3][j2][r] + bias[by * 64 + j2];
+    t[((size_t)b * 8 + r) * 256 + by * 64 + j2] += v;
+  }
+}
+
+__global__ __launch_bounds__(256) void cross_attn_ln_kernel(
+    const float* __restrict__ t, const float* __restrict__ nw, const float* __restrict__ nb,
+    const float* __restrict__ cqw, const float* __restrict__ cqb,
+    const unsigned short* __restrict__ KV, int koff, int voff, float* __restrict__ out) {
+  __shared__ float X[256];
+  __shared__ float sv[512];
+  __shared__ float red[256];
+  __shared__ float qv[32];
+  __shared__ float pvred[8][32];
+  __shared__ float sred[4], vred[4];
+  int tid = threadIdx.x;
+  int bid = blockIdx.x;
+  int q = bid % KQ;
+  int h = (bid / KQ) % H;
+  int b = bid / (KQ * H);
+  {
+    float v = t[((size_t)(b * KQ + q)) * 256 + tid];
+    int lane = tid & 63, w = tid >> 6;
+    float s = v;
+    #pragma unroll
+    for (int off = 32; off > 0; off >>= 1) s += __shfl_xor(s, off);
+    if (lane == 0) sred[w] = s;
+    __syncthreads();
+    float mean = (sred[0] + sred[1] + sred[2] + sred[3]) * (1.f / 256);
+    float d = v - mean;
+    float vr = d * d;
+    #pragma unroll
+    for (int off = 32; off > 0; off >>= 1) vr += __shfl_xor(vr, off);
+    if (lane == 0) vred[w] = vr;
+    __syncthreads();
+    float inv = rsqrtf((vred[0] + vred[1] + vred[2] + vred[3]) * (1.f / 256) + 1e-5f);
+    X[tid] = d * inv * nw[tid] + nb[tid];
+  }
+  __syncthreads();
+  {
+    int dd = tid >> 3, part = tid & 7;
+    int col = h * HD + dd;
+    const float4* wp = (const float4*)(cqw + (size_t)col * 256 + part * 32);
+    float acc = 0.f;
+    #pragma unroll
+    for (int kk = 0; kk < 8; ++kk) {
+      float4 wv = wp[kk];
+      float4 xv = *(const float4*)&X[part * 32 + kk * 4];
+      acc += xv.x * wv.x + xv.y * wv.y + xv.z * wv.z + xv.w * wv.w;
+    }
+    red[tid] = acc;
+  }
+  __syncthreads();
+  if (tid < 32) {
+    float acc = 0.f;
+    #pragma unroll
+    for (int p = 0; p < 8; ++p) acc += red[tid * 8 + p];
+    qv[tid] = acc + cqb[h * HD + tid];
+  }
+  __syncthreads();
+  const float scale = 0.17677669529663687f;
+  for (int k = tid; k < SEQ; k += 256) {
+    const unsigned short* kp = KV + ((size_t)(b * SEQ + k)) * 1536 + koff + h * HD;
+    float d = 0.f;
+    #pragma unroll
+    for (int j4 = 0; j4 < 4; ++j4) {
+      s8b kv8 = *(const s8b*)(kp + j4 * 8);
+      #pragma unroll
+      for (int j = 0; j < 8; ++j)
+        d += qv[j4 * 8 + j] * b2f((unsigned short)kv8[j]);
+    }
+    sv[k] = d * scale;
+  }
+  __syncthreads();
+  float m = -1e30f;
+  for (int k = tid; k < SEQ; k += 256) m = fmaxf(m, sv[k]);
+  red[tid] = m; __syncthreads();
+  for (int s = 128; s > 0; s >>= 1) {
+    if (tid < s) red[tid] = fmaxf(red[tid], red[tid + s]);
+    __syncthreads();
+  }
+  m = red[0]; __syncthreads();
+  float lsum = 0.f;
+  for (int k = tid; k < SEQ; k += 256) { float e = __expf(sv[k] - m); sv[k] = e; lsum += e; }
+  red[tid] = lsum; __syncthreads();
+  for (int s = 128; s > 0; s >>= 1) {
+    if (tid < s) red[tid] += red[tid + s];
+    __syncthreads();
+  }
+  float denom = red[0];
+  int d = tid & 31, g = tid >> 5;
+  float acc = 0.f;
+  for (int k = g; k < SEQ; k += 8)
+    acc += sv[k] * b2f(KV[((size_t)(b * SEQ + k)) * 1536 + voff + h * HD + d]);
+  pvred[g][d] = acc;
+  __syncthreads();
+  if (tid < 32) {
+    float r = 0.f;
+    #pragma unroll
+    for (int gg = 0; gg < 8; ++gg) r += pvred[gg][tid];
+    out[((size_t)(b * KQ + q)) * E + h * HD + tid] = r / denom;
+  }
 }
 
 __global__ __launch_bounds__(256) void pool_gather_kernel(
@@ -760,8 +832,7 @@
   float* attnout_d = h + (size_t)ROWS * E;
   float* pg        = attnout_d + (size_t)TROWS * E;
   float* tbuf      = pg + BATCH * 2 * E;
-  float* q_t       = tbuf + (size_t)TROWS * E;
-  float* qkv_t     = q_t + (size_t)TROWS * E;
+  float* qkv_t     = tbuf + (size_t)TROWS * E;
   float* dmid      = qkv_t + (size_t)TROWS * 3 * E;
   float* kvb3      = dmid + (size_t)TROWS * FF;
   unsigned short* kv_bf   = (unsigned short*)(kvb3 + 1536);
@@ -777,34 +848,32 @@
   unsigned short* qkb = mid_bf;
   unsigned short* vtb = mid_bf + (size_t)2 * ROWS * E;
 
-  auto cvt = [&](const float* src, unsigned short* dst, size_t n) {
-    int n4 = (int)(n / 4);
-    f2b_kernel<<<(n4 + 255) / 256, 256, 0, stream>>>(src, dst, n4);
-  };
-
-  cvt(e_qkv_w, eqkv_bf, (size_t)LE * 3 * E * E);
-  cvt(e_out_w, eout_bf, (size_t)LE * E * E);
-  cvt(e_l1_w, el1_bf, (size_t)LE * FF * E);
-  cvt(e_l2_w, el2_bf, (size_t)LE * E * FF);
+  {
+    const int total_quads = (LE * 3 * E * E + LE * E * E + LE * FF * E + LE * E * FF) / 4;
+    cvt_all_kernel<<<(total_quads + 255) / 256, 256, 0, stream>>>(
+        e_qkv_w, e_out_w, e_l1_w, e_l2_w, eqkv_bf, eout_bf, el1_bf, el2_bf);
+  }
   kvw_remap_kernel<<<384, 256, 0, stream>>>(d_cqkv_w, d_cqkv_b, kvw_bf, kvb3);
   coords_kernel<<<(BATCH * SEQ + 255) / 256, 256, 0, stream>>>(x, carr);
 
-  input_proj_kernel<<<ROWS, 256, 0, stream>>>(x, in_w, in_b, bn_w, bn_b, h);
+  input_proj_ln_kernel<<<ROWS, 256, 0, stream>>>(x, in_w, in_b, bn_w, bn_b,
+                                                 e_n1_w, e_n1_b, h, hn_bf);
 
   for (int i = 0; i < LE; ++i) {
     const float* qb = e_qkv_b + (size_t)i * 3 * E;
     const float* ob = e_out_b + (size_t)i * E;
     const float* l1b = e_l1_b + (size_t)i * FF;
     const float* l2b = e_l2_b + (size_t)i * E;
-    ln_bf16_kernel<<<ROWS, 64, 0, stream>>>(h, e_n1_w + i * E, e_n1_b + i * E, hn_bf);
-    mfma_gemm_kernel<0, 0, 2><<<dim3(6, 64), 256, 0, stream>>>(
-        hn_bf, eqkv_bf + (size_t)i * 3 * E * E, qb, nullptr, nullptr, qkb, vtb, ROWS, 3 * E, E);
+    if (i > 0)
+      ln_bf16_kernel<<<ROWS, 64, 0, stream>>>(h, e_n1_w + i * E, e_n1_b + i * E, hn_bf);
+    mfma_gemm64o_kernel<0, 2><<<dim3(6, 128), 256, 0, stream>>>(
+        hn_bf, eqkv_bf + (size_t)i * 3 * E * E, qb, qkb, vtb, 3 * E, E);
     mfma_attn_kernel<<<dim3(SEQ / 64, H, BATCH), 256, 0, stream>>>(qkb, vtb, carr, dr_gamma, attn_bf);
     mfma_gemm64_kernel<<<dim3(2, 128), 256, 0, stream>>>(
         attn_bf, eout_bf + (size_t)i * E * E, ob, h, h, ROWS, E, E);
     ln_bf16_kernel<<<ROWS, 64, 0, stream>>>(h, e_n2_w + i * E, e_n2_b + i * E, hn_bf);
-    mfma_gemm_kernel<1, 0, 1><<<dim3(8, 64), 256, 0, stream>>>(
-        hn_bf, el1_bf + (size_t)i * FF * E, l1b, nullptr, nullptr, mid_bf, nullptr, ROWS, FF, E);
+    mfma_gemm64o_kernel<1, 1><<<dim3(8, 128), 256, 0, stream>>>(
+        hn_bf, el1_bf + (size_t)i * FF * E, l1b, mid_bf, nullptr, FF, E);
     mfma_gemm64_kernel<<<dim3(2, 128), 256, 0, stream>>>(
         mid_bf, el2_bf + (size_t)i * E * FF, l2b, h, h, ROWS, E, FF);
   }
@@ -814,9 +883,9 @@
   pool_gather_kernel<<<dim3(BATCH, 8), 256, 0, stream>>>(h, parent_idx, pg);
   cond_kernel<<<BATCH, 256, 0, stream>>>(pg, c1_w, c1_b, c2_w, c2_b, query_embed, tbuf);
 
-  cvt(h, hn_bf, (size_t)ROWS * E);
-  mfma_gemm_kernel<0, 0, 1><<<dim3(12, 64), 256, 0, stream>>>(
-      hn_bf, kvw_bf, kvb3, nullptr, nullptr, kv_bf, nullptr, ROWS, 3 * E * 2, E);
+  f2b_kernel<<<(ROWS * E / 4 + 255) / 256, 256, 0, stream>>>(h, hn_bf, ROWS * E / 4);
+  mfma_gemm64o_kernel<0, 1><<<dim3(12, 128), 256, 0, stream>>>(
+      hn_bf, kvw_bf, kvb3, kv_bf, nullptr, 3 * E * 2, E);
 
   for (int i = 0; i < LDN; ++i) {
     dec_ln_gemv_kernel<768, 0><<<dim3(BATCH, 12), 256, 0, stream>>>(
@@ -824,11 +893,10 @@
         d_sqkv_w + (size_t)i * 3 * E * E, d_sqkv_b + (size_t)i * 3 * E, qkv_t);
     dec_selfattn_sout_kernel<<<dim3(BATCH, 4), 256, 0, stream>>>(
         qkv_t, d_sout_w + (size_t)i * E * E, d_sout_b + (size_t)i * E, tbuf);
-    dec_ln_gemv_kernel<256, 0><<<dim3(BATCH, 4), 256, 0, stream>>>(
+    cross_attn_ln_kernel<<<BATCH * H * KQ, 256, 0, stream>>>(
         tbuf, d_n2_w + i * E, d_n2_b + i * E,
-        d_cqkv_w + (size_t)i * 3 * E * E, d_cqkv_b + (size_t)i * 3 * E, q_t);
-    cross_attn_kernel<<<BATCH * H * KQ, 256, 0, stream>>>(
-        q_t, kv_bf, i * 512, i * 512 + 256, attnout_d);
+        d_cqkv_w + (size_t)i * 3 * E * E, d_cqkv_b + (size_t)i * 3 * E,
+        kv_bf, i * 512, i * 512 + 256, attnout_d);
     dec_gemv_resid_kernel<<<dim3(BATCH, 4), 256, 0, stream>>>(
         attnout_d, d_cout_w + (size_t)i * E * E, d_cout_b + (size_t)i * E, tbuf);
     dec_ln_gemv_kernel<1024, 1><<<dim3(BATCH, 16), 256, 0, stream>>>(
```

After: 757.7 us. -5.9%, faster.
